# Performance work log

Hardware: AMD Instinct MI355X
Metric: run time of the kernel (lower is better)

Reference implementation:

```python
import jax, jax.numpy as jnp
import numpy as np

K = 9
DILATION = 1
EPS = 1e-12  # F.normalize eps


def setup_inputs() -> dict:
    key = jax.random.key(0)
    x = jax.random.normal(key, (2, 192, 8192, 1), dtype=jnp.float32)
    return {"x": x}


def reference(x):
    # x: [B, C, N, 1]
    # L2-normalize along channel dim (dim=1), like F.normalize(x, p=2, dim=1)
    norm = jnp.sqrt(jnp.sum(x * x, axis=1, keepdims=True))
    xn = x / jnp.maximum(norm, EPS)
    # -> [B, N, C]
    pts = jnp.squeeze(xn, -1).transpose(0, 2, 1)
    B, N, C = pts.shape
    kk = K * DILATION
    # pairwise squared distance: ||xi||^2 - 2 xi.xj + ||xj||^2  -> [B, N, N]
    sq = jnp.sum(pts * pts, axis=-1)  # [B, N]
    inner = jnp.einsum('bnc,bmc->bnm', pts, pts)
    dist = sq[:, :, None] - 2.0 * inner + sq[:, None, :]
    # topk of -dist == k nearest neighbors
    _, nn_idx = jax.lax.top_k(-dist, kk)  # [B, N, kk] int32
    nn_idx = nn_idx.astype(jnp.int64) if False else nn_idx
    center_idx = jnp.broadcast_to(jnp.arange(N, dtype=nn_idx.dtype)[None, :, None], (B, N, kk))
    edge_index = jnp.stack((nn_idx, center_idx), axis=0)  # [2, B, N, kk]
    # dilation slicing
    return edge_index[:, :, :, ::DILATION]
```

## Files before the change

kernel.cpp:

```cpp
#include <hip/hip_runtime.h>
#include <math.h>

#define BATCH 2
#define CH    192
#define NPTS  8192
#define KNN   9

#define NT     64
#define TLIST  8
#define NT32   256
#define KS     12
#define CSPLIT 16
#define NITER  (NT32 / CSPLIT)
#define NCANDP 256
#define P2ROWS 4
#define NSEL   12

typedef __attribute__((ext_vector_type(8)))  short  bf16x8;
typedef __attribute__((ext_vector_type(8)))  unsigned short u16x8;
typedef __attribute__((ext_vector_type(16))) float  f32x16;

static __device__ __forceinline__ unsigned short f2bf(float f) {
    unsigned u = __float_as_uint(f);
    u += 0x7fffu + ((u >> 16) & 1u);
    return (unsigned short)(u >> 16);
}
static __device__ __forceinline__ bf16x8 negbf(bf16x8 v) {
    bf16x8 r;
    #pragma unroll
    for (int e = 0; e < 8; ++e) r[e] = (short)(v[e] ^ (short)0x8000);
    return r;
}
static __device__ __forceinline__ unsigned umax2(unsigned a, unsigned b) {
    return a > b ? a : b;
}
static __device__ __forceinline__ unsigned umin2(unsigned a, unsigned b) {
    return a < b ? a : b;
}

__global__ __launch_bounds__(256) void knn_normalize(
    const float* __restrict__ x,
    unsigned short* __restrict__ pk, float* __restrict__ x_rm,
    double* __restrict__ rdnd, double* __restrict__ ssd)
{
    __shared__ float  tile[CH][NT + 1];
    __shared__ double rdn_sh[NT];

    const int b   = blockIdx.x >> 7;
    const int rb  = blockIdx.x & 127;
    const int n0  = rb << 6;
    const int tid = threadIdx.x;
    const float* xb = x + (size_t)b * CH * NPTS;

    #pragma unroll
    for (int i = 0; i < (CH * NT) / 256; ++i) {
        int flat = tid + i * 256;
        int c = flat >> 6, j = flat & 63;
        tile[c][j] = xb[(size_t)c * NPTS + n0 + j];
    }
    __syncthreads();

    {
        const int j = tid >> 2, q = tid & 3;
        double ss = 0.0;
        #pragma unroll 8
        for (int c = 0; c < 48; ++c) {
            double v = (double)tile[q * 48 + c][j];
            ss = fma(v, v, ss);
        }
        ss += __shfl_xor(ss, 1, 64);
        ss += __shfl_xor(ss, 2, 64);
        if (q == 0) {
            double dn = sqrt(ss);
            if (dn < 1e-12) dn = 1e-12;
            double rdn = 1.0 / dn;
            rdn_sh[j] = rdn;
            rdnd[b * NPTS + n0 + j] = rdn;
            ssd [b * NPTS + n0 + j] = ss;
        }
    }
    __syncthreads();

    #pragma unroll
    for (int i = 0; i < 6; ++i) {
        int pid  = tid + i * 256;
        int frag = pid >> 6;
        int lane = pid & 63;
        int tl   = frag / KS;
        int ks   = frag - tl * KS;
        int rl   = (tl << 5) + (lane & 31);
        int kb   = (ks << 4) + ((lane >> 5) << 3);
        double rdn = rdn_sh[rl];
        u16x8 hv;
        #pragma unroll
        for (int e = 0; e < 8; ++e) {
            float v = (float)((double)tile[kb + e][rl] * rdn);
            hv[e] = f2bf(v);
        }
        size_t base = ((size_t)((b * NT32 + (rb << 1) + tl) * KS + ks)) * 512
                      + ((size_t)lane << 3);
        *(u16x8*)(pk + base) = hv;
    }

    #pragma unroll
    for (int i = 0; i < (CH * NT) / 256; ++i) {
        int flat = tid + i * 256;
        int j = flat / CH, c = flat - j * CH;
        x_rm[(size_t)(b * NPTS + n0 + j) * CH + c] = tile[c][j];
    }
}

__global__ __attribute__((amdgpu_flat_work_group_size(256, 256),
                          amdgpu_waves_per_eu(4, 4)))
void knn_phase1(
    const unsigned short* __restrict__ pk,
    unsigned* __restrict__ cand_p)
{
    const int bid  = blockIdx.x;
    const int b    = bid >> 10;
    const int r10  = bid & 1023;
    const int qb   = r10 >> 4;
    const int cs   = r10 & 15;
    const int tid  = threadIdx.x;
    const int wave = tid >> 6;
    const int lane = tid & 63;
    const unsigned short* pkb = pk + (size_t)b * (NT32 * KS * 512);

    const int qt = qb * 4 + wave;
    bf16x8 qf[KS];
    #pragma unroll
    for (int ks = 0; ks < KS; ++ks) {
        const unsigned short* p = pkb + ((size_t)(qt * KS + ks)) * 512 + (lane << 3);
        qf[ks] = negbf(*(const bf16x8*)p);
    }
    #pragma unroll
    for (int ks = 0; ks < KS; ++ks)
        asm volatile("" : "+a"(qf[ks]));

    unsigned lst[TLIST];
    #pragma unroll
    for (int t = 0; t < TLIST; ++t) lst[t] = 0xFFFFFF00u | t;

    const unsigned short* gbase = pkb + (size_t)(cs * NITER) * (KS * 512) + (lane << 3);

    for (int it = 0; it < NITER; ++it) {
        const unsigned short* gt = gbase + (size_t)it * (KS * 512);

        f32x16 acc;
        #pragma unroll
        for (int r = 0; r < 16; ++r) acc[r] = 4.f;

        #pragma unroll
        for (int ks = 0; ks < KS; ++ks) {
            bf16x8 cf = *(const bf16x8*)(gt + (ks << 9));
            acc = __builtin_amdgcn_mfma_f32_32x32x16_bf16(cf, qf[ks], acc, 0, 0, 0);
        }

        const unsigned pb = (unsigned)(it << 4);
        #pragma unroll
        for (int r = 0; r < 16; ++r) {
            unsigned hi = (__float_as_uint(acc[r]) & 0xFFFFFF00u) | pb | (unsigned)r;
            #pragma unroll
            for (int t = 0; t < TLIST; ++t) {
                unsigned lo = umin2(lst[t], hi);
                hi = umax2(lst[t], hi);
                lst[t] = lo;
            }
        }
        asm volatile("" : "+v"(lst[0]), "+v"(lst[1]), "+v"(lst[2]), "+v"(lst[3]),
                          "+v"(lst[4]), "+v"(lst[5]), "+v"(lst[6]), "+v"(lst[7]));
    }

    const int query = (qt << 5) + (lane & 31);
    const int h     = lane >> 5;
    unsigned* dst = cand_p + ((size_t)(b * NPTS + query) << 8) + (cs << 4) + (h << 3);
    uint4 w0 = make_uint4(lst[0], lst[1], lst[2], lst[3]);
    uint4 w1 = make_uint4(lst[4], lst[5], lst[6], lst[7]);
    *(uint4*)dst       = w0;
    *(uint4*)(dst + 4) = w1;
}

__global__ __launch_bounds__(256) void knn_phase2(
    const float* __restrict__ x_rm,
    const double* __restrict__ rdnd, const double* __restrict__ ssd,
    const unsigned* __restrict__ cand_p,
    int* __restrict__ out)
{
    __shared__ double xc[P2ROWS][CH];
    __shared__ int    sel[P2ROWS][16];
    __shared__ double dks[P2ROWS][16];

    const int bi   = blockIdx.x;
    const int b    = bi >> 11;
    const int r0   = (bi & 2047) << 2;
    const int tid  = threadIdx.x;
    const int wave = tid >> 6;
    const int lane = tid & 63;
    const int bN   = b * NPTS;

    for (int i = tid; i < P2ROWS * CH; i += 256) {
        int r = i / CH, c = i - r * CH;
        xc[r][c] = (double)x_rm[(size_t)(bN + r0 + r) * CH + c] * rdnd[bN + r0 + r];
    }
    __syncthreads();

    const int row = r0 + wave;

    unsigned long long qq[4];
    {
        uint4 pv = *(const uint4*)(cand_p + ((size_t)(bN + row) << 8) + (lane << 2));
        unsigned pk4[4] = {pv.x, pv.y, pv.z, pv.w};
        #pragma unroll
        for (int u = 0; u < 4; ++u) {
            int f = (lane << 2) + u;
            int cs = f >> 4, h = (f >> 3) & 1;
            unsigned pkv = pk4[u];
            int r = (int)(pkv & 15u), ct = (int)((pkv >> 4) & 15u);
            int rowc = (r & 3) + ((r >> 2) << 3) + (h << 2);
            int col  = (cs << 9) + (ct << 5) + rowc;
            qq[u] = ((unsigned long long)pkv << 32) | (unsigned)col;
        }
        unsigned long long t;
        #define CE(a, b) if (qq[b] < qq[a]) { t = qq[a]; qq[a] = qq[b]; qq[b] = t; }
        CE(0,1) CE(2,3) CE(0,2) CE(1,3) CE(1,2)
        #undef CE
    }

    unsigned long long my_sel = 0;
    #pragma unroll
    for (int round = 0; round < NSEL; ++round) {
        unsigned long long m = qq[0];
        #pragma unroll
        for (int off = 1; off < 64; off <<= 1) {
            unsigned long long o = __shfl_xor(m, off, 64);
            m = (o < m) ? o : m;
        }
        if (qq[0] == m) {
            qq[0] = qq[1]; qq[1] = qq[2]; qq[2] = qq[3];
            qq[3] = 0xFFFFFFFFFFFFFFFFull;
        }
        if (lane == round) my_sel = m;
    }
    if (lane < NSEL) sel[wave][lane] = (int)((unsigned)my_sel & 0x3FFFu);
    __builtin_amdgcn_wave_barrier();

    {
        const int c = lane & 15, qd = lane >> 4;
        if (c < NSEL) {
            const int m = sel[wave][c];
            const double rdm = rdnd[bN + m];
            const float* xr = x_rm + (size_t)(bN + m) * CH + qd * 48;
            const double* xcp = &xc[wave][qd * 48];
            double s0 = 0.0, s1 = 0.0, s2 = 0.0, s3 = 0.0;
            #pragma unroll
            for (int j = 0; j < 12; ++j) {
                float4 v = *(const float4*)(xr + (j << 2));
                s0 = fma((double)v.x * rdm, xcp[(j << 2) + 0], s0);
                s1 = fma((double)v.y * rdm, xcp[(j << 2) + 1], s1);
                s2 = fma((double)v.z * rdm, xcp[(j << 2) + 2], s2);
                s3 = fma((double)v.w * rdm, xcp[(j << 2) + 3], s3);
            }
            double dot = (s0 + s1) + (s2 + s3);
            dot += __shfl_xor(dot, 16, 64);
            dot += __shfl_xor(dot, 32, 64);
            if (qd == 0) dks[wave][c] = fma(-2.0, dot, ssd[bN + m] * rdm * rdm);
        } else {
            double dot = 0.0;
            dot += __shfl_xor(dot, 16, 64);
            dot += __shfl_xor(dot, 32, 64);
        }
    }
    __builtin_amdgcn_wave_barrier();

    if (lane == 0) {
        const int n = row;
        unsigned used = 0;
        for (int k = 0; k < KNN; ++k) {
            double bd = INFINITY; int bm = 0x7fffffff; int bp = 0;
            #pragma unroll
            for (int s = 0; s < NSEL; ++s) {
                if (!((used >> s) & 1u)) {
                    double d = dks[wave][s]; int m = sel[wave][s];
                    if (d < bd || (d == bd && m < bm)) { bd = d; bm = m; bp = s; }
                }
            }
            used |= (1u << bp);
            out[(size_t)(bN + n) * KNN + k] = bm;
            out[(size_t)BATCH * NPTS * KNN + (size_t)(bN + n) * KNN + k] = n;
        }
    }
}

extern "C" void kernel_launch(void* const* d_in, const int* in_sizes, int n_in,
                              void* d_out, int out_size, void* d_ws, size_t ws_size,
                              hipStream_t stream)
{
    const float* x = (const float*)d_in[0];
    int* out = (int*)d_out;

    char* ws = (char*)d_ws;
    const size_t sz_pk  = (size_t)BATCH * NT32 * KS * 512 * sizeof(unsigned short);
    const size_t sz_xrm = (size_t)BATCH * NPTS * CH * sizeof(float);
    const size_t sz_rdn = (size_t)BATCH * NPTS * sizeof(double);
    const size_t sz_ss  = sz_rdn;

    unsigned short* pk = (unsigned short*)(ws);
    float*  x_rm   = (float*) (ws + sz_pk);
    double* rdnd   = (double*)(ws + sz_pk + sz_xrm);
    double* ssd    = (double*)(ws + sz_pk + sz_xrm + sz_rdn);
    unsigned* cand_p = (unsigned*)(ws + sz_pk + sz_xrm + sz_rdn + sz_ss);

    knn_normalize<<<BATCH * (NPTS / NT), 256, 0, stream>>>(x, pk, x_rm, rdnd, ssd);
    knn_phase1  <<<BATCH * 64 * CSPLIT, 256, 0, stream>>>(pk, cand_p);
    knn_phase2  <<<BATCH * (NPTS / P2ROWS), 256, 0, stream>>>(x_rm, rdnd, ssd, cand_p, out);
}
```

Baseline: 161.3 us.

## Split MFMA accumulator chain, lower phase1 occupancy, parallelize final top-k selection

Phase 1 now uses two independent MFMA accumulator chains that are summed at the end, which shortens the dependent MFMA chain. The occupancy hint drops from 4 to 3 waves per EU so the extra accumulator registers fit. The final selection of the 9 nearest neighbours out of 12 candidates no longer runs serially in lane 0; each of 12 lanes computes its candidate's rank in parallel and writes directly. Adding the two partial sums can change bf16/fp32 rounding slightly, which may alter candidate ordering near ties.

```diff
diff --git a/kernel.cpp b/kernel.cpp
--- a/kernel.cpp
+++ b/kernel.cpp
@@ -111,7 +111,7 @@
 }
 
 __global__ __attribute__((amdgpu_flat_work_group_size(256, 256),
-                          amdgpu_waves_per_eu(4, 4)))
+                          amdgpu_waves_per_eu(3, 3)))
 void knn_phase1(
     const unsigned short* __restrict__ pk,
     unsigned* __restrict__ cand_p)
@@ -146,20 +146,23 @@
     for (int it = 0; it < NITER; ++it) {
         const unsigned short* gt = gbase + (size_t)it * (KS * 512);
 
-        f32x16 acc;
-        #pragma unroll
-        for (int r = 0; r < 16; ++r) acc[r] = 4.f;
-
-        #pragma unroll
-        for (int ks = 0; ks < KS; ++ks) {
-            bf16x8 cf = *(const bf16x8*)(gt + (ks << 9));
-            acc = __builtin_amdgcn_mfma_f32_32x32x16_bf16(cf, qf[ks], acc, 0, 0, 0);
+        f32x16 acc0, acc1;
+        #pragma unroll
+        for (int r = 0; r < 16; ++r) { acc0[r] = 4.f; acc1[r] = 0.f; }
+
+        #pragma unroll
+        for (int ks = 0; ks < KS; ks += 2) {
+            bf16x8 cf0 = *(const bf16x8*)(gt + (ks << 9));
+            bf16x8 cf1 = *(const bf16x8*)(gt + ((ks + 1) << 9));
+            acc0 = __builtin_amdgcn_mfma_f32_32x32x16_bf16(cf0, qf[ks],     acc0, 0, 0, 0);
+            acc1 = __builtin_amdgcn_mfma_f32_32x32x16_bf16(cf1, qf[ks + 1], acc1, 0, 0, 0);
         }
 
         const unsigned pb = (unsigned)(it << 4);
         #pragma unroll
         for (int r = 0; r < 16; ++r) {
-            unsigned hi = (__float_as_uint(acc[r]) & 0xFFFFFF00u) | pb | (unsigned)r;
+            unsigned hi = (__float_as_uint(acc0[r] + acc1[r]) & 0xFFFFFF00u)
+                          | pb | (unsigned)r;
             #pragma unroll
             for (int t = 0; t < TLIST; ++t) {
                 unsigned lo = umin2(lst[t], hi);
@@ -272,21 +275,19 @@
     }
     __builtin_amdgcn_wave_barrier();
 
-    if (lane == 0) {
-        const int n = row;
-        unsigned used = 0;
-        for (int k = 0; k < KNN; ++k) {
-            double bd = INFINITY; int bm = 0x7fffffff; int bp = 0;
-            #pragma unroll
-            for (int s = 0; s < NSEL; ++s) {
-                if (!((used >> s) & 1u)) {
-                    double d = dks[wave][s]; int m = sel[wave][s];
-                    if (d < bd || (d == bd && m < bm)) { bd = d; bm = m; bp = s; }
-                }
-            }
-            used |= (1u << bp);
-            out[(size_t)(bN + n) * KNN + k] = bm;
-            out[(size_t)BATCH * NPTS * KNN + (size_t)(bN + n) * KNN + k] = n;
+    if (lane < NSEL) {
+        const double dm = dks[wave][lane];
+        const int    sm = sel[wave][lane];
+        int cnt = 0;
+        #pragma unroll
+        for (int s = 0; s < NSEL; ++s) {
+            double d = dks[wave][s]; int m = sel[wave][s];
+            cnt += (d < dm || (d == dm && m < sm)) ? 1 : 0;
+        }
+        if (cnt < KNN) {
+            const int n = row;
+            out[(size_t)(bN + n) * KNN + cnt] = sm;
+            out[(size_t)BATCH * NPTS * KNN + (size_t)(bN + n) * KNN + cnt] = n;
         }
     }
 }
```

After: 160.7 us. About the same (-0.4%).
